# Kernel tuning notes

Hardware: AMD Instinct MI355X
Metric: run time of the kernel (lower is better)

## Reference

```python
import jax, jax.numpy as jnp
import numpy as np

N_NODES = 100000
SIG_DIM = 64
N_ADJ = 1600000
N_QUERY = 262144


def setup_inputs() -> dict:
    key = jax.random.key(0)
    k1, k2, k3, k4, k5 = jax.random.split(key, 5)
    x = jax.random.normal(k1, (N_NODES, SIG_DIM), dtype=jnp.float32)
    x = x / jnp.linalg.norm(x, axis=1, keepdims=True)  # F.normalize(p=2, dim=1)
    node_weight = jax.random.uniform(k2, (N_NODES,), dtype=jnp.float32)
    edges = jax.random.randint(k3, (2, N_QUERY), 0, N_NODES)
    adj_row = jnp.sort(jax.random.randint(k4, (N_ADJ,), 0, N_NODES))
    adj_col = jax.random.randint(k5, (N_ADJ,), 0, N_NODES)
    return {
        "x": x,
        "node_weight": node_weight,
        "edges": edges,
        "adj_row": adj_row,
        "adj_col": adj_col,
        "num_nodes": N_NODES,
    }


def reference(x, node_weight, edges, adj_row, adj_col, num_nodes):
    # node signatures scaled by node weight
    xw = x * node_weight[:, None]                      # [N, D]

    seg = lambda vals: jax.ops.segment_sum(vals, adj_row, num_segments=num_nodes)

    # SpMM propagation: (A @ x)[i] = sum_{j in N(i)} x[j]
    one_hop = seg(xw[adj_col])                          # [N, D]
    deg = seg(jnp.ones_like(adj_row, dtype=xw.dtype))   # [N]
    two_iter = seg(one_hop[adj_col])                    # [N, D]

    # combine mode
    two_hop = two_iter - one_hop - xw
    deg2 = jnp.maximum(seg(deg[adj_col]) - deg - 1.0, 0.0)

    row, col = edges[0], edges[1]
    x_u_1 = one_hop[row]
    x_v_1 = one_hop[col]
    x_u_2 = two_hop[row]
    x_v_2 = two_hop[col]

    dot = lambda a, b: (a * b).sum(axis=-1)

    deg_u = deg[row]
    deg_v = deg[col]
    deg_u_2 = deg2[row]
    deg_v_2 = deg2[col]

    count_1_1 = dot(x_u_1, x_v_1)
    count_1_2 = dot(x_u_1, x_v_2)
    count_2_1 = dot(x_u_2, x_v_1)
    count_2_2 = dot(x_u_2, x_v_2)
    count_1_inf = deg_u + deg_v - 2 * count_1_1 - count_1_2 - count_2_1
    count_2_inf = deg_u_2 + deg_v_2 - 2 * count_2_2 - count_1_2 - count_2_1

    x_u_iter = two_iter[row]
    x_v_iter = two_iter[col]
    x_u = xw[row]
    x_v = xw[col]
    comb_count_1_2 = dot(x_u_1, x_v_iter)
    comb_count_2_1 = dot(x_u_iter, x_v_1)
    comb_count_2_2 = dot(x_u_iter - deg_u[:, None] * x_u,
                         x_v_iter - deg_v[:, None] * x_v)
    comb_count_self_1_2 = dot(x_u_1, x_u_iter)
    comb_count_self_2_1 = dot(x_v_1, x_v_iter)

    features = jnp.stack([
        count_1_1, count_1_2, count_2_1, count_2_2,
        count_1_inf, count_2_inf,
        comb_count_1_2, comb_count_2_1, comb_count_2_2,
        comb_count_self_1_2, comb_count_self_2_1,
        deg_u, deg_v, deg_u_2, deg_v_2,
    ], axis=1)                                          # [E, 15]
    return features
```

## Files before the change

### kernel.cpp

```cpp
#include <hip/hip_runtime.h>


#define D 64

typedef unsigned int uint32;

__device__ __forceinline__ uint32 pack2(float a, float b) {
    uint32 ua = __float_as_uint(a);
    ua += 0x7fffu + ((ua >> 16) & 1u);
    uint32 ub = __float_as_uint(b);
    ub += 0x7fffu + ((ub >> 16) & 1u);
    return (ua >> 16) | (ub & 0xffff0000u);
}
__device__ __forceinline__ float lo2f(uint32 u) { return __uint_as_float(u << 16); }
__device__ __forceinline__ float hi2f(uint32 u) { return __uint_as_float(u & 0xffff0000u); }

#define RED_GRP(v)  { v += __shfl_xor(v, 1, 64); v += __shfl_xor(v, 2, 64);  v += __shfl_xor(v, 4, 64);  }

__global__ void __launch_bounds__(256) prep_kernel(const float4* __restrict__ x,
                                                   const float* __restrict__ w,
                                                   uint4* __restrict__ xw,
                                                   const int* __restrict__ adj_row,
                                                   int* __restrict__ row_ptr,
                                                   int n8, int n, int nadj, int xw_blocks) {
    if ((int)blockIdx.x < xw_blocks) {
        int i = blockIdx.x * blockDim.x + threadIdx.x;
        if (i >= n8) return;
        float s = w[i >> 3];
        float4 a = x[i * 2], b = x[i * 2 + 1];
        uint4 o;
        o.x = pack2(a.x * s, a.y * s);
        o.y = pack2(a.z * s, a.w * s);
        o.z = pack2(b.x * s, b.y * s);
        o.w = pack2(b.z * s, b.w * s);
        xw[i] = o;
    } else {
        int i = (blockIdx.x - xw_blocks) * blockDim.x + threadIdx.x;
        if (i > n) return;
        int lo = 0, hi = nadj;
        while (lo < hi) {
            int mid = (lo + hi) >> 1;
            if (adj_row[mid] < i) lo = mid + 1; else hi = mid;
        }
        row_ptr[i] = lo;
    }
}

template <bool WITH_DEG2>
__global__ void __launch_bounds__(256) spmm_kernel(const uint4* __restrict__ src,
                                                   const int* __restrict__ row_ptr,
                                                   const int* __restrict__ adj_col,
                                                   const float* __restrict__ degv,
                                                   uint4* __restrict__ dst,
                                                   float* __restrict__ degout,
                                                   float2* __restrict__ degpair,
                                                   int n) {
    int lane = threadIdx.x & 63;
    int sub = lane & 7;
    int node = blockIdx.x * 32 + (threadIdx.x >> 6) * 8 + (lane >> 3);
    if (node >= n) return;
    int start = row_ptr[node], end = row_ptr[node + 1];
    int deg_n = end - start;
    float a0 = 0.f, a1 = 0.f, a2 = 0.f, a3 = 0.f,
          a4 = 0.f, a5 = 0.f, a6 = 0.f, a7 = 0.f;
    float dsum = 0.f;
    int gbase = lane & 56;
    const int* colp = adj_col + start;
    int base = 0;
    for (; base + 8 <= deg_n; base += 8) {
        int idx = colp[base + sub];
        if (WITH_DEG2) dsum += degv[idx];
#pragma unroll
        for (int i = 0; i < 8; ++i) {
            int c = __shfl(idx, gbase + i, 64);
            uint4 qv = src[(size_t)c * 8 + sub];
            a0 += lo2f(qv.x); a1 += hi2f(qv.x);
            a2 += lo2f(qv.y); a3 += hi2f(qv.y);
            a4 += lo2f(qv.z); a5 += hi2f(qv.z);
            a6 += lo2f(qv.w); a7 += hi2f(qv.w);
        }
    }
    if (base < deg_n) {
        int k = base + sub;
        bool kv = k < deg_n;
        int idx = kv ? colp[k] : 0;
        if (WITH_DEG2) { if (kv) dsum += degv[idx]; }
#pragma unroll
        for (int i = 0; i < 8; ++i) {
            if (base + i < deg_n) {
                int c = __shfl(idx, gbase + i, 64);
                uint4 qv = src[(size_t)c * 8 + sub];
                a0 += lo2f(qv.x); a1 += hi2f(qv.x);
                a2 += lo2f(qv.y); a3 += hi2f(qv.y);
                a4 += lo2f(qv.z); a5 += hi2f(qv.z);
                a6 += lo2f(qv.w); a7 += hi2f(qv.w);
            }
        }
    }
    uint4 o;
    o.x = pack2(a0, a1); o.y = pack2(a2, a3);
    o.z = pack2(a4, a5); o.w = pack2(a6, a7);
    dst[(size_t)node * 8 + sub] = o;
    if (WITH_DEG2) {
        RED_GRP(dsum)
        if (sub == 0)
            degpair[node] = make_float2((float)deg_n,
                                        fmaxf(dsum - (float)deg_n - 1.0f, 0.0f));
    } else {
        if (sub == 0) degout[node] = (float)deg_n;
    }
}

__global__ void __launch_bounds__(256) edge_kernel(const int* __restrict__ edges,
                                                   const uint4* __restrict__ xw,
                                                   const uint4* __restrict__ h1,
                                                   const uint4* __restrict__ t2,
                                                   const float2* __restrict__ degpair,
                                                   float* __restrict__ out,
                                                   int E) {
    int t = blockIdx.x * blockDim.x + threadIdx.x;
    int q = t >> 3, sub = t & 7;
    if (q >= E) return;
    int u = edges[q], v = edges[E + q];
    uint4 pxu = xw[(size_t)u * 8 + sub], pxv = xw[(size_t)v * 8 + sub];
    uint4 phu = h1[(size_t)u * 8 + sub], phv = h1[(size_t)v * 8 + sub];
    uint4 ptu = t2[(size_t)u * 8 + sub], ptv = t2[(size_t)v * 8 + sub];
    float2 dpu = degpair[u], dpv = degpair[v];
    float du = dpu.x, du2 = dpu.y, dv = dpv.x, dv2 = dpv.y;

    float c11 = 0.f, c12 = 0.f, c21 = 0.f, c22 = 0.f,
          cc12 = 0.f, cc21 = 0.f, cc22 = 0.f, cs12 = 0.f, cs21 = 0.f;

    uint32 axu[4] = {pxu.x, pxu.y, pxu.z, pxu.w};
    uint32 axv[4] = {pxv.x, pxv.y, pxv.z, pxv.w};
    uint32 ahu[4] = {phu.x, phu.y, phu.z, phu.w};
    uint32 ahv[4] = {phv.x, phv.y, phv.z, phv.w};
    uint32 atu[4] = {ptu.x, ptu.y, ptu.z, ptu.w};
    uint32 atv[4] = {ptv.x, ptv.y, ptv.z, ptv.w};

    auto accum = [&](float xu, float xv, float hu, float hv, float tu, float tv) {
        float h2u = tu - hu - xu, h2v = tv - hv - xv;
        float au = fmaf(-du, xu, tu), av = fmaf(-dv, xv, tv);
        c11  = fmaf(hu,  hv,  c11);
        c12  = fmaf(hu,  h2v, c12);
        c21  = fmaf(h2u, hv,  c21);
        c22  = fmaf(h2u, h2v, c22);
        cc12 = fmaf(hu,  tv,  cc12);
        cc21 = fmaf(tu,  hv,  cc21);
        cc22 = fmaf(au,  av,  cc22);
        cs12 = fmaf(hu,  tu,  cs12);
        cs21 = fmaf(hv,  tv,  cs21);
    };
#pragma unroll
    for (int k = 0; k < 4; ++k) {
        accum(lo2f(axu[k]), lo2f(axv[k]), lo2f(ahu[k]), lo2f(ahv[k]), lo2f(atu[k]), lo2f(atv[k]));
        accum(hi2f(axu[k]), hi2f(axv[k]), hi2f(ahu[k]), hi2f(ahv[k]), hi2f(atu[k]), hi2f(atv[k]));
    }
    RED_GRP(c11) RED_GRP(c12) RED_GRP(c21) RED_GRP(c22)
    RED_GRP(cc12) RED_GRP(cc21) RED_GRP(cc22) RED_GRP(cs12) RED_GRP(cs21)

    if (sub == 0) {
        float* o = out + (size_t)q * 15;
        o[0]  = c11;
        o[1]  = c12;
        o[2]  = c21;
        o[3]  = c22;
        o[4]  = du + dv - 2.f * c11 - c12 - c21;
        o[5]  = du2 + dv2 - 2.f * c22 - c12 - c21;
        o[6]  = cc12;
        o[7]  = cc21;
        o[8]  = cc22;
        o[9]  = cs12;
        o[10] = cs21;
        o[11] = du;
        o[12] = dv;
        o[13] = du2;
        o[14] = dv2;
    }
}

extern "C" void kernel_launch(void* const* d_in, const int* in_sizes, int n_in,
                              void* d_out, int out_size, void* d_ws, size_t ws_size,
                              hipStream_t stream) {
    const float* x       = (const float*)d_in[0];
    const float* w       = (const float*)d_in[1];
    const int*   edges   = (const int*)d_in[2];
    const int*   adj_row = (const int*)d_in[3];
    const int*   adj_col = (const int*)d_in[4];

    const int N    = in_sizes[1];
    const int E    = in_sizes[2] / 2;
    const int NADJ = in_sizes[3];

    char* ws = (char*)d_ws;
    size_t off = 0;
    auto take = [&](size_t bytes) {
        void* p = ws + off;
        off = (off + bytes + 255) & ~(size_t)255;
        return p;
    };
    uint4*  xw      = (uint4*)take((size_t)N * D * 2);
    uint4*  one_hop = (uint4*)take((size_t)N * D * 2);
    uint4*  two_it  = (uint4*)take((size_t)N * D * 2);
    float*  deg     = (float*)take((size_t)N * sizeof(float));
    float2* degpair = (float2*)take((size_t)N * sizeof(float2));
    int*    row_ptr = (int*)take((size_t)(N + 1) * sizeof(int));
    (void)ws_size;

    float* out = (float*)d_out;

    {
        int n8 = N * 8;
        int xw_blocks = (n8 + 255) / 256;
        int rp_blocks = (N + 1 + 255) / 256;
        prep_kernel<<<xw_blocks + rp_blocks, 256, 0, stream>>>(
            (const float4*)x, w, xw, adj_row, row_ptr, n8, N, NADJ, xw_blocks);
    }
    spmm_kernel<false><<<(N + 31) / 32, 256, 0, stream>>>(xw, row_ptr, adj_col, nullptr,
                                                          one_hop, deg, nullptr, N);
    spmm_kernel<true><<<(N + 31) / 32, 256, 0, stream>>>(one_hop, row_ptr, adj_col, deg,
                                                         two_it, nullptr, degpair, N);
    edge_kernel<<<((size_t)E * 8 + 255) / 256, 256, 0, stream>>>(edges, xw, one_hop, two_it,
                                                                 degpair, out, E);
}
```

Before: 188.9 us.

## Fuse all stages into one cooperative persistent kernel with grid syncs

Replaces the four separate launches (prep, two SpMM passes, edge features) with one cooperative kernel. It loops over tiles persistently and uses grid-wide barriers between stages, sized from occupancy with 256 CUs assumed. This is meant to remove per-launch overhead and inter-kernel gaps. In exchange it adds grid.sync costs, can lose occupancy because __launch_bounds__(256,8) limits registers, and removes the tail overlap the hardware scheduler gave across separate kernels.

```diff
diff --git a/kernel.cpp b/kernel.cpp
--- a/kernel.cpp
+++ b/kernel.cpp
@@ -1,4 +1,7 @@
 #include <hip/hip_runtime.h>
+#include <hip/hip_cooperative_groups.h>
+
+namespace cg = cooperative_groups;
 
 
 #define D 64
@@ -17,47 +20,20 @@
 
 #define RED_GRP(v)  { v += __shfl_xor(v, 1, 64); v += __shfl_xor(v, 2, 64);  v += __shfl_xor(v, 4, 64);  }
 
-__global__ void __launch_bounds__(256) prep_kernel(const float4* __restrict__ x,
-                                                   const float* __restrict__ w,
-                                                   uint4* __restrict__ xw,
-                                                   const int* __restrict__ adj_row,
-                                                   int* __restrict__ row_ptr,
-                                                   int n8, int n, int nadj, int xw_blocks) {
-    if ((int)blockIdx.x < xw_blocks) {
-        int i = blockIdx.x * blockDim.x + threadIdx.x;
-        if (i >= n8) return;
-        float s = w[i >> 3];
-        float4 a = x[i * 2], b = x[i * 2 + 1];
-        uint4 o;
-        o.x = pack2(a.x * s, a.y * s);
-        o.y = pack2(a.z * s, a.w * s);
-        o.z = pack2(b.x * s, b.y * s);
-        o.w = pack2(b.z * s, b.w * s);
-        xw[i] = o;
-    } else {
-        int i = (blockIdx.x - xw_blocks) * blockDim.x + threadIdx.x;
-        if (i > n) return;
-        int lo = 0, hi = nadj;
-        while (lo < hi) {
-            int mid = (lo + hi) >> 1;
-            if (adj_row[mid] < i) lo = mid + 1; else hi = mid;
-        }
-        row_ptr[i] = lo;
-    }
-}
 
 template <bool WITH_DEG2>
-__global__ void __launch_bounds__(256) spmm_kernel(const uint4* __restrict__ src,
-                                                   const int* __restrict__ row_ptr,
-                                                   const int* __restrict__ adj_col,
-                                                   const float* __restrict__ degv,
-                                                   uint4* __restrict__ dst,
-                                                   float* __restrict__ degout,
-                                                   float2* __restrict__ degpair,
-                                                   int n) {
-    int lane = threadIdx.x & 63;
+__device__ __forceinline__ void spmm_tile(int vb, int tid,
+                                          const uint4* __restrict__ src,
+                                          const int* __restrict__ row_ptr,
+                                          const int* __restrict__ adj_col,
+                                          const float* __restrict__ degv,
+                                          uint4* __restrict__ dst,
+                                          float* __restrict__ degout,
+                                          float2* __restrict__ degpair,
+                                          int n) {
+    int lane = tid & 63;
     int sub = lane & 7;
-    int node = blockIdx.x * 32 + (threadIdx.x >> 6) * 8 + (lane >> 3);
+    int node = vb * 32 + (tid >> 6) * 8 + (lane >> 3);
     if (node >= n) return;
     int start = row_ptr[node], end = row_ptr[node + 1];
     int deg_n = end - start;
@@ -111,14 +87,15 @@
     }
 }
 
-__global__ void __launch_bounds__(256) edge_kernel(const int* __restrict__ edges,
-                                                   const uint4* __restrict__ xw,
-                                                   const uint4* __restrict__ h1,
-                                                   const uint4* __restrict__ t2,
-                                                   const float2* __restrict__ degpair,
-                                                   float* __restrict__ out,
-                                                   int E) {
-    int t = blockIdx.x * blockDim.x + threadIdx.x;
+__device__ __forceinline__ void edge_tile(int vb, int tid,
+                                          const int* __restrict__ edges,
+                                          const uint4* __restrict__ xw,
+                                          const uint4* __restrict__ h1,
+                                          const uint4* __restrict__ t2,
+                                          const float2* __restrict__ degpair,
+                                          float* __restrict__ out,
+                                          int E) {
+    int t = vb * 256 + tid;
     int q = t >> 3, sub = t & 7;
     if (q >= E) return;
     int u = edges[q], v = edges[E + q];
@@ -179,6 +156,67 @@
     }
 }
 
+
+__global__ void __launch_bounds__(256, 8)
+fused_kernel(const float4* __restrict__ x, const float* __restrict__ w,
+             const int* __restrict__ edges,
+             const int* __restrict__ adj_row, const int* __restrict__ adj_col,
+             uint4* __restrict__ xw, uint4* __restrict__ one_hop,
+             uint4* __restrict__ two_it,
+             float* __restrict__ deg, float2* __restrict__ degpair,
+             int* __restrict__ row_ptr, float* __restrict__ out,
+             int N, int E, int NADJ) {
+    cg::grid_group grid = cg::this_grid();
+    const int tid = threadIdx.x;
+    const int nb = gridDim.x;
+    const int gstride = nb * 256;
+
+    {
+        int n8 = N * 8;
+        for (int i = blockIdx.x * 256 + tid; i < n8; i += gstride) {
+            float s = w[i >> 3];
+            float4 a = x[i * 2], b = x[i * 2 + 1];
+            uint4 o;
+            o.x = pack2(a.x * s, a.y * s);
+            o.y = pack2(a.z * s, a.w * s);
+            o.z = pack2(b.x * s, b.y * s);
+            o.w = pack2(b.z * s, b.w * s);
+            xw[i] = o;
+        }
+        for (int i = blockIdx.x * 256 + tid; i <= N; i += gstride) {
+            int lo = 0, hi = NADJ;
+            while (lo < hi) {
+                int mid = (lo + hi) >> 1;
+                if (adj_row[mid] < i) lo = mid + 1; else hi = mid;
+            }
+            row_ptr[i] = lo;
+        }
+    }
+    grid.sync();
+
+    {
+        int tiles = (N + 31) / 32;
+        for (int vb = blockIdx.x; vb < tiles; vb += nb)
+            spmm_tile<false>(vb, tid, xw, row_ptr, adj_col, nullptr,
+                             one_hop, deg, nullptr, N);
+    }
+    grid.sync();
+
+    {
+        int tiles = (N + 31) / 32;
+        for (int vb = blockIdx.x; vb < tiles; vb += nb)
+            spmm_tile<true>(vb, tid, one_hop, row_ptr, adj_col, deg,
+                            two_it, nullptr, degpair, N);
+    }
+    grid.sync();
+
+    {
+        int tiles = (int)(((size_t)E * 8 + 255) / 256);
+        for (int vb = blockIdx.x; vb < tiles; vb += nb)
+            edge_tile(vb, tid, edges, xw, one_hop, two_it, degpair, out, E);
+    }
+}
+
 extern "C" void kernel_launch(void* const* d_in, const int* in_sizes, int n_in,
                               void* d_out, int out_size, void* d_ws, size_t ws_size,
                               hipStream_t stream) {
@@ -209,17 +247,21 @@
 
     float* out = (float*)d_out;
 
-    {
-        int n8 = N * 8;
-        int xw_blocks = (n8 + 255) / 256;
-        int rp_blocks = (N + 1 + 255) / 256;
-        prep_kernel<<<xw_blocks + rp_blocks, 256, 0, stream>>>(
-            (const float4*)x, w, xw, adj_row, row_ptr, n8, N, NADJ, xw_blocks);
-    }
-    spmm_kernel<false><<<(N + 31) / 32, 256, 0, stream>>>(xw, row_ptr, adj_col, nullptr,
-                                                          one_hop, deg, nullptr, N);
-    spmm_kernel<true><<<(N + 31) / 32, 256, 0, stream>>>(one_hop, row_ptr, adj_col, deg,
-                                                         two_it, nullptr, degpair, N);
-    edge_kernel<<<((size_t)E * 8 + 255) / 256, 256, 0, stream>>>(edges, xw, one_hop, two_it,
-                                                                 degpair, out, E);
-}
+    int blocksPerCU = 0;
+    (void)hipOccupancyMaxActiveBlocksPerMultiprocessor(&blocksPerCU,
+                                                       (const void*)fused_kernel, 256, 0);
+    if (blocksPerCU < 1) blocksPerCU = 1;
+    long long grid = (long long)blocksPerCU * 256;
+    long long maxTiles = ((long long)E * 8 + 255) / 256;
+    long long tilesN = (N + 31) / 32;
+    if (maxTiles < tilesN) maxTiles = tilesN;
+    if (grid > maxTiles) grid = maxTiles;
+
+    const float4* x4 = (const float4*)x;
+    void* args[] = {(void*)&x4, (void*)&w, (void*)&edges, (void*)&adj_row,
+                    (void*)&adj_col, (void*)&xw, (void*)&one_hop, (void*)&two_it,
+                    (void*)&deg, (void*)&degpair, (void*)&row_ptr, (void*)&out,
+                    (void*)&N, (void*)&E, (void*)&NADJ};
+    hipLaunchCooperativeKernel((void*)fused_kernel, dim3((unsigned)grid), dim3(256),
+                               args, 0, stream);
+}
```

New measurement: 593.7 us. 3.14x slower.

## Store weighted node signatures as scaled FP8 and accumulate first hop in FP16

Applied to the files above, without the earlier changes.

The weighted signatures xw are pre-scaled by 64 and packed as 8-bit e4m3-style values, halving their footprint relative to bf16. A bit-shift decoder turns each byte pair into FP16, with the exponent offset folding away the scale. The first SpMM accumulates with packed FP16 adds, and the edge kernel also reads the FP8 xw. This cuts gather bandwidth in the first propagation and the edge pass. The cost is much coarser precision (3-bit mantissa, approximate subnormals, clamping at the top of the range) plus FP16 accumulation, which may break accuracy tolerance.

```diff
diff --git a/kernel.cpp b/kernel.cpp
--- a/kernel.cpp
+++ b/kernel.cpp
@@ -4,6 +4,10 @@
 #define D 64
 
 typedef unsigned int uint32;
+typedef _Float16 h2 __attribute__((ext_vector_type(2)));
+
+union U32H2 { uint32 u; h2 h; };
+__device__ __forceinline__ h2 u_as_h2(uint32 u) { U32H2 t; t.u = u; return t.h; }
 
 __device__ __forceinline__ uint32 pack2(float a, float b) {
     uint32 ua = __float_as_uint(a);
@@ -15,25 +19,49 @@
 __device__ __forceinline__ float lo2f(uint32 u) { return __uint_as_float(u << 16); }
 __device__ __forceinline__ float hi2f(uint32 u) { return __uint_as_float(u & 0xffff0000u); }
 
+__device__ __forceinline__ uint32 enc1(float v) {
+    float a = fabsf(v);
+    uint32 s = (__float_as_uint(v) >> 24) & 0x80u;
+    if (a >= 448.f) return s | 0x7Eu;
+    if (a < 0.015625f) {
+        uint32 m = (uint32)rintf(a * 512.f);
+        return (m > 7u) ? (s | 0x08u) : (s | m);
+    }
+    uint32 b = __float_as_uint(a);
+    b += 0x7FFFFu + ((b >> 20) & 1u);
+    uint32 m3 = (b >> 20) & 7u;
+    int e4 = (int)(b >> 23) - 127 + 7;
+    if (e4 > 15) return s | 0x7Eu;
+    return s | ((uint32)e4 << 3) | m3;
+}
+
+__device__ __forceinline__ void dec8(uint32 u, uint32& pe, uint32& po) {
+    uint32 se = (u << 8) & 0x80008000u;
+    uint32 ue = u & 0x007f007fu;
+    pe = ((ue << 7) + 0x08000800u) | se;
+    uint32 so = u & 0x80008000u;
+    uint32 uo = (u >> 8) & 0x007f007fu;
+    po = ((uo << 7) + 0x08000800u) | so;
+}
+
 #define RED_GRP(v)  { v += __shfl_xor(v, 1, 64); v += __shfl_xor(v, 2, 64);  v += __shfl_xor(v, 4, 64);  }
 
 __global__ void __launch_bounds__(256) prep_kernel(const float4* __restrict__ x,
                                                    const float* __restrict__ w,
-                                                   uint4* __restrict__ xw,
+                                                   uint2* __restrict__ xw,
                                                    const int* __restrict__ adj_row,
                                                    int* __restrict__ row_ptr,
                                                    int n8, int n, int nadj, int xw_blocks) {
     if ((int)blockIdx.x < xw_blocks) {
         int i = blockIdx.x * blockDim.x + threadIdx.x;
         if (i >= n8) return;
-        float s = w[i >> 3];
+        float s = w[i >> 3] * 64.f;
         float4 a = x[i * 2], b = x[i * 2 + 1];
-        uint4 o;
-        o.x = pack2(a.x * s, a.y * s);
-        o.y = pack2(a.z * s, a.w * s);
-        o.z = pack2(b.x * s, b.y * s);
-        o.w = pack2(b.z * s, b.w * s);
-        xw[i] = o;
+        uint32 w0 = enc1(a.x * s) | (enc1(a.z * s) << 8)
+                  | (enc1(a.y * s) << 16) | (enc1(a.w * s) << 24);
+        uint32 w1 = enc1(b.x * s) | (enc1(b.z * s) << 8)
+                  | (enc1(b.y * s) << 16) | (enc1(b.w * s) << 24);
+        xw[i] = make_uint2(w0, w1);
     } else {
         int i = (blockIdx.x - xw_blocks) * blockDim.x + threadIdx.x;
         if (i > n) return;
@@ -46,15 +74,67 @@
     }
 }
 
-template <bool WITH_DEG2>
-__global__ void __launch_bounds__(256) spmm_kernel(const uint4* __restrict__ src,
-                                                   const int* __restrict__ row_ptr,
-                                                   const int* __restrict__ adj_col,
-                                                   const float* __restrict__ degv,
-                                                   uint4* __restrict__ dst,
-                                                   float* __restrict__ degout,
-                                                   float2* __restrict__ degpair,
-                                                   int n) {
+__global__ void __launch_bounds__(256) spmm1_kernel(const uint2* __restrict__ src,
+                                                    const int* __restrict__ row_ptr,
+                                                    const int* __restrict__ adj_col,
+                                                    uint4* __restrict__ dst,
+                                                    float* __restrict__ degout,
+                                                    int n) {
+    int lane = threadIdx.x & 63;
+    int sub = lane & 7;
+    int node = blockIdx.x * 32 + (threadIdx.x >> 6) * 8 + (lane >> 3);
+    if (node >= n) return;
+    int start = row_ptr[node], end = row_ptr[node + 1];
+    int deg_n = end - start;
+    h2 acc0 = u_as_h2(0u), acc1 = u_as_h2(0u), acc2 = u_as_h2(0u), acc3 = u_as_h2(0u);
+    int gbase = lane & 56;
+    const int* colp = adj_col + start;
+    int base = 0;
+    for (; base + 8 <= deg_n; base += 8) {
+        int idx = colp[base + sub];
+#pragma unroll
+        for (int i = 0; i < 8; ++i) {
+            int c = __shfl(idx, gbase + i, 64);
+            uint2 qv = src[(size_t)c * 8 + sub];
+            uint32 pe, po;
+            dec8(qv.x, pe, po);
+            acc0 += u_as_h2(pe); acc1 += u_as_h2(po);
+            dec8(qv.y, pe, po);
+            acc2 += u_as_h2(pe); acc3 += u_as_h2(po);
+        }
+    }
+    if (base < deg_n) {
+        int k = base + sub;
+        int idx = (k < deg_n) ? colp[k] : 0;
+#pragma unroll
+        for (int i = 0; i < 8; ++i) {
+            if (base + i < deg_n) {
+                int c = __shfl(idx, gbase + i, 64);
+                uint2 qv = src[(size_t)c * 8 + sub];
+                uint32 pe, po;
+                dec8(qv.x, pe, po);
+                acc0 += u_as_h2(pe); acc1 += u_as_h2(po);
+                dec8(qv.y, pe, po);
+                acc2 += u_as_h2(pe); acc3 += u_as_h2(po);
+            }
+        }
+    }
+    uint4 o;
+    o.x = pack2((float)acc0.x, (float)acc0.y);
+    o.y = pack2((float)acc1.x, (float)acc1.y);
+    o.z = pack2((float)acc2.x, (float)acc2.y);
+    o.w = pack2((float)acc3.x, (float)acc3.y);
+    dst[(size_t)node * 8 + sub] = o;
+    if (sub == 0) degout[node] = (float)deg_n;
+}
+
+__global__ void __launch_bounds__(256) spmm2_kernel(const uint4* __restrict__ src,
+                                                    const int* __restrict__ row_ptr,
+                                                    const int* __restrict__ adj_col,
+                                                    const float* __restrict__ degv,
+                                                    uint4* __restrict__ dst,
+                                                    float2* __restrict__ degpair,
+                                                    int n) {
     int lane = threadIdx.x & 63;
     int sub = lane & 7;
     int node = blockIdx.x * 32 + (threadIdx.x >> 6) * 8 + (lane >> 3);
@@ -69,7 +149,7 @@
     int base = 0;
     for (; base + 8 <= deg_n; base += 8) {
         int idx = colp[base + sub];
-        if (WITH_DEG2) dsum += degv[idx];
+        dsum += degv[idx];
 #pragma unroll
         for (int i = 0; i < 8; ++i) {
             int c = __shfl(idx, gbase + i, 64);
@@ -84,7 +164,7 @@
         int k = base + sub;
         bool kv = k < deg_n;
         int idx = kv ? colp[k] : 0;
-        if (WITH_DEG2) { if (kv) dsum += degv[idx]; }
+        if (kv) dsum += degv[idx];
 #pragma unroll
         for (int i = 0; i < 8; ++i) {
             if (base + i < deg_n) {
@@ -101,18 +181,14 @@
     o.x = pack2(a0, a1); o.y = pack2(a2, a3);
     o.z = pack2(a4, a5); o.w = pack2(a6, a7);
     dst[(size_t)node * 8 + sub] = o;
-    if (WITH_DEG2) {
-        RED_GRP(dsum)
-        if (sub == 0)
-            degpair[node] = make_float2((float)deg_n,
-                                        fmaxf(dsum - (float)deg_n - 1.0f, 0.0f));
-    } else {
-        if (sub == 0) degout[node] = (float)deg_n;
-    }
+    RED_GRP(dsum)
+    if (sub == 0)
+        degpair[node] = make_float2((float)deg_n,
+                                    fmaxf(dsum - (float)deg_n - 1.0f, 0.0f));
 }
 
 __global__ void __launch_bounds__(256) edge_kernel(const int* __restrict__ edges,
-                                                   const uint4* __restrict__ xw,
+                                                   const uint2* __restrict__ xw,
                                                    const uint4* __restrict__ h1,
                                                    const uint4* __restrict__ t2,
                                                    const float2* __restrict__ degpair,
@@ -122,23 +198,44 @@
     int q = t >> 3, sub = t & 7;
     if (q >= E) return;
     int u = edges[q], v = edges[E + q];
-    uint4 pxu = xw[(size_t)u * 8 + sub], pxv = xw[(size_t)v * 8 + sub];
+    uint2 pxu = xw[(size_t)u * 8 + sub], pxv = xw[(size_t)v * 8 + sub];
     uint4 phu = h1[(size_t)u * 8 + sub], phv = h1[(size_t)v * 8 + sub];
     uint4 ptu = t2[(size_t)u * 8 + sub], ptv = t2[(size_t)v * 8 + sub];
     float2 dpu = degpair[u], dpv = degpair[v];
     float du = dpu.x, du2 = dpu.y, dv = dpv.x, dv2 = dpv.y;
 
+    float fxu[8], fxv[8], fhu[8], fhv[8], ftu[8], ftv[8];
+    {
+        uint32 pe, po;
+        dec8(pxu.x, pe, po);
+        h2 e = u_as_h2(pe), o_ = u_as_h2(po);
+        fxu[0] = (float)e.x; fxu[1] = (float)e.y; fxu[2] = (float)o_.x; fxu[3] = (float)o_.y;
+        dec8(pxu.y, pe, po);
+        e = u_as_h2(pe); o_ = u_as_h2(po);
+        fxu[4] = (float)e.x; fxu[5] = (float)e.y; fxu[6] = (float)o_.x; fxu[7] = (float)o_.y;
+        dec8(pxv.x, pe, po);
+        e = u_as_h2(pe); o_ = u_as_h2(po);
+        fxv[0] = (float)e.x; fxv[1] = (float)e.y; fxv[2] = (float)o_.x; fxv[3] = (float)o_.y;
+        dec8(pxv.y, pe, po);
+        e = u_as_h2(pe); o_ = u_as_h2(po);
+        fxv[4] = (float)e.x; fxv[5] = (float)e.y; fxv[6] = (float)o_.x; fxv[7] = (float)o_.y;
+    }
+    fhu[0]=lo2f(phu.x); fhu[1]=hi2f(phu.x); fhu[2]=lo2f(phu.y); fhu[3]=hi2f(phu.y);
+    fhu[4]=lo2f(phu.z); fhu[5]=hi2f(phu.z); fhu[6]=lo2f(phu.w); fhu[7]=hi2f(phu.w);
+    fhv[0]=lo2f(phv.x); fhv[1]=hi2f(phv.x); fhv[2]=lo2f(phv.y); fhv[3]=hi2f(phv.y);
+    fhv[4]=lo2f(phv.z); fhv[5]=hi2f(phv.z); fhv[6]=lo2f(phv.w); fhv[7]=hi2f(phv.w);
+    ftu[0]=lo2f(ptu.x); ftu[1]=hi2f(ptu.x); ftu[2]=lo2f(ptu.y); ftu[3]=hi2f(ptu.y);
+    ftu[4]=lo2f(ptu.z); ftu[5]=hi2f(ptu.z); ftu[6]=lo2f(ptu.w); ftu[7]=hi2f(ptu.w);
+    ftv[0]=lo2f(ptv.x); ftv[1]=hi2f(ptv.x); ftv[2]=lo2f(ptv.y); ftv[3]=hi2f(ptv.y);
+    ftv[4]=lo2f(ptv.z); ftv[5]=hi2f(ptv.z); ftv[6]=lo2f(ptv.w); ftv[7]=hi2f(ptv.w);
+
     float c11 = 0.f, c12 = 0.f, c21 = 0.f, c22 = 0.f,
           cc12 = 0.f, cc21 = 0.f, cc22 = 0.f, cs12 = 0.f, cs21 = 0.f;
-
-    uint32 axu[4] = {pxu.x, pxu.y, pxu.z, pxu.w};
-    uint32 axv[4] = {pxv.x, pxv.y, pxv.z, pxv.w};
-    uint32 ahu[4] = {phu.x, phu.y, phu.z, phu.w};
-    uint32 ahv[4] = {phv.x, phv.y, phv.z, phv.w};
-    uint32 atu[4] = {ptu.x, ptu.y, ptu.z, ptu.w};
-    uint32 atv[4] = {ptv.x, ptv.y, ptv.z, ptv.w};
-
-    auto accum = [&](float xu, float xv, float hu, float hv, float tu, float tv) {
+#pragma unroll
+    for (int j = 0; j < 8; ++j) {
+        float xu = fxu[j], xv = fxv[j];
+        float hu = fhu[j], hv = fhv[j];
+        float tu = ftu[j], tv = ftv[j];
         float h2u = tu - hu - xu, h2v = tv - hv - xv;
         float au = fmaf(-du, xu, tu), av = fmaf(-dv, xv, tv);
         c11  = fmaf(hu,  hv,  c11);
@@ -150,11 +247,6 @@
         cc22 = fmaf(au,  av,  cc22);
         cs12 = fmaf(hu,  tu,  cs12);
         cs21 = fmaf(hv,  tv,  cs21);
-    };
-#pragma unroll
-    for (int k = 0; k < 4; ++k) {
-        accum(lo2f(axu[k]), lo2f(axv[k]), lo2f(ahu[k]), lo2f(ahv[k]), lo2f(atu[k]), lo2f(atv[k]));
-        accum(hi2f(axu[k]), hi2f(axv[k]), hi2f(ahu[k]), hi2f(ahv[k]), hi2f(atu[k]), hi2f(atv[k]));
     }
     RED_GRP(c11) RED_GRP(c12) RED_GRP(c21) RED_GRP(c22)
     RED_GRP(cc12) RED_GRP(cc21) RED_GRP(cc22) RED_GRP(cs12) RED_GRP(cs21)
@@ -199,7 +291,7 @@
         off = (off + bytes + 255) & ~(size_t)255;
         return p;
     };
-    uint4*  xw      = (uint4*)take((size_t)N * D * 2);
+    uint2*  xw      = (uint2*)take((size_t)N * 8 * sizeof(uint2));
     uint4*  one_hop = (uint4*)take((size_t)N * D * 2);
     uint4*  two_it  = (uint4*)take((size_t)N * D * 2);
     float*  deg     = (float*)take((size_t)N * sizeof(float));
@@ -216,10 +308,9 @@
         prep_kernel<<<xw_blocks + rp_blocks, 256, 0, stream>>>(
             (const float4*)x, w, xw, adj_row, row_ptr, n8, N, NADJ, xw_blocks);
     }
-    spmm_kernel<false><<<(N + 31) / 32, 256, 0, stream>>>(xw, row_ptr, adj_col, nullptr,
-                                                          one_hop, deg, nullptr, N);
-    spmm_kernel<true><<<(N + 31) / 32, 256, 0, stream>>>(one_hop, row_ptr, adj_col, deg,
-                                                         two_it, nullptr, degpair, N);
+    spmm1_kernel<<<(N + 31) / 32, 256, 0, stream>>>(xw, row_ptr, adj_col, one_hop, deg, N);
+    spmm2_kernel<<<(N + 31) / 32, 256, 0, stream>>>(one_hop, row_ptr, adj_col, deg,
+                                                    two_it, degpair, N);
     edge_kernel<<<((size_t)E * 8 + 255) / 256, 256, 0, stream>>>(edges, xw, one_hop, two_it,
                                                                  degpair, out, E);
 }
```

Result: no change. 186.2 us (-1.4%).
